# Optimization experiments

Measured on AMD Instinct MI355X. Metric: run time of the kernel, lower is better.

Reference implementation:

```python
import jax, jax.numpy as jnp
import numpy as np
from jax import lax

B = 2048
C = 8
H = W = 14
NP = H * W  # 196
DIM = 192
THETA = 0.7


def _unfold3(z):
    # z: [B, C, H, W] -> patches [B, C, 9, H, W], matching F.unfold(kernel=3, pad=1)
    p = jnp.pad(z, ((0, 0), (0, 0), (1, 1), (1, 1)))
    return jnp.stack([p[:, :, dy:dy + H, dx:dx + W]
                      for dy in range(3) for dx in range(3)], axis=2)


def setup_inputs() -> dict:
    key = jax.random.key(0)
    ks = jax.random.split(key, 10)
    s = 0.1
    return {
        "x": jax.random.normal(ks[0], (B, 1 + NP, DIM), dtype=jnp.float32),
        "W1": jax.random.normal(ks[1], (C, DIM), dtype=jnp.float32) * s,      # linear1 192->8
        "b1": jax.random.normal(ks[2], (C,), dtype=jnp.float32) * s,
        "conv1_w": jax.random.normal(ks[3], (C, C), dtype=jnp.float32) * s,   # 1x1 conv
        "conv1_b": jax.random.normal(ks[4], (C,), dtype=jnp.float32) * s,
        "cdc_w": jax.random.normal(ks[5], (C, C, 1, 5), dtype=jnp.float32) * s,
        "wc1": jax.random.normal(ks[6], (C, C), dtype=jnp.float32) * s,       # WConv1 (1x1)
        "wc2": jax.random.normal(ks[7], (C, C), dtype=jnp.float32) * s,       # WConv2 (1x1)
        "hist_w": jax.random.normal(ks[8], (DIM, C), dtype=jnp.float32) * s,  # linear 8->192
        "hist_b": jax.random.normal(ks[9], (DIM,), dtype=jnp.float32) * s,
    }


def reference(x, W1, b1, conv1_w, conv1_b, cdc_w, wc1, wc2, hist_w, hist_b):
    class_token, tok = x[:, :1, :], x[:, 1:, :]
    # linear1: [B,196,192] -> [B,196,8]
    t = jnp.einsum('bnd,cd->bnc', tok, W1) + b1
    # -> [B,8,14,14]
    t = t.reshape(-1, H, W, C).transpose(0, 3, 1, 2)

    # conv1 (1x1)
    x1 = jnp.einsum('bihw,oi->bohw', t, conv1_w) + conv1_b[None, :, None, None]

    # CDC: scatter the 1x5 weights into a 3x3 cross-shaped kernel
    w5 = cdc_w[:, :, 0, :]  # [O,I,5]
    z = jnp.zeros((C, C, 1), dtype=cdc_w.dtype)
    k9 = jnp.concatenate([z, w5[:, :, 0:1], z,
                          w5[:, :, 1:2], w5[:, :, 2:3], w5[:, :, 3:4],
                          z, w5[:, :, 4:5], z], axis=2).reshape(C, C, 3, 3)
    out_normal = lax.conv_general_dilated(
        t, k9, window_strides=(1, 1), padding=((1, 1), (1, 1)),
        dimension_numbers=('NCHW', 'OIHW', 'NCHW'))
    kernel_diff = cdc_w.sum(axis=(2, 3))  # [O,I]
    out_diff = jnp.einsum('bihw,oi->bohw', t, kernel_diff)
    x2 = out_normal - THETA * out_diff

    z_star = x1 + x2  # [B,8,14,14]

    # TokenHistogram
    mu = jnp.einsum('bihw,oi->bohw', z_star, wc1)
    gamma = jnp.einsum('bihw,oi->bohw', z_star, wc2)
    zp = _unfold3(z_star)   # [B,8,9,14,14]
    mp = _unfold3(mu)
    gp = _unfold3(gamma)
    u = gp * (zp - mp)
    z_hist = jnp.exp(-u * u).sum(axis=2) / 9.0  # [B,8,14,14]
    # torch .reshape(-1, NP, 8): plain row-major reshape (mixes C and HW)
    z_hist = z_hist.reshape(-1, NP, C)
    y = jnp.einsum('bnc,dc->bnd', z_hist, hist_w) + hist_b  # [B,196,192]

    return jnp.concatenate([class_token, y], axis=1)
```

## Files before the change

kernel.cpp:

```cpp
#include <hip/hip_runtime.h>


#define DIMD 192

__launch_bounds__(256)
__global__ void sadapter_kernel(
    const float* __restrict__ x,
    const float* __restrict__ W1,
    const float* __restrict__ b1,
    const float* __restrict__ conv1_w,
    const float* __restrict__ conv1_b,
    const float* __restrict__ cdc_w,
    const float* __restrict__ wc1,
    const float* __restrict__ wc2,
    const float* __restrict__ hist_w,
    const float* __restrict__ hist_b,
    float* __restrict__ out)
{
    __shared__ float smem[4608];
    float* TS  = smem;
    float* ZH  = smem;
    float* PS  = smem + 2048;
    float* WB2 = smem + 4096;

    const int tid = threadIdx.x;
    const float* xb   = x   + (size_t)blockIdx.x * (197 * DIMD);
    float*       outb = out + (size_t)blockIdx.x * (197 * DIMD);

    {
        float4 z4 = make_float4(0.f, 0.f, 0.f, 0.f);
        float4 o4 = make_float4(1.f, 1.f, 1.f, 1.f);
        ((float4*)TS)[tid]       = z4;
        ((float4*)TS)[tid + 256] = z4;
        ((float4*)PS)[tid]       = o4;
        ((float4*)PS)[tid + 256] = o4;
    }
    if (tid < 64) {
        const float* c5 = cdc_w + tid * 5;
        float k0 = c5[0], k1 = c5[1], k2 = c5[2], k3 = c5[3], k4 = c5[4];
        float kd = k0 + k1 + k2 + k3 + k4;
        float* wp = WB2 + tid * 8;
        wp[0] = conv1_w[tid] + k2 - 0.7f * kd;
        wp[1] = k0; wp[2] = k1; wp[3] = k3; wp[4] = k4;
        wp[5] = wc1[tid];
        wp[6] = wc2[tid];
        wp[7] = 0.f;
    }
    __syncthreads();

    if (tid < 196) {
        const float4* rowp = (const float4*)(xb + DIMD + tid * DIMD);
        float acc[8];
        #pragma unroll
        for (int c = 0; c < 8; ++c) acc[c] = b1[c];
        #pragma unroll
        for (int blk = 0; blk < 6; ++blk) {
            float4 tv[8];
            #pragma unroll
            for (int u = 0; u < 8; ++u) tv[u] = rowp[blk * 8 + u];
            #pragma unroll
            for (int c = 0; c < 8; ++c) {
                const float* wrow = W1 + c * DIMD + blk * 32;
                #pragma unroll
                for (int u = 0; u < 8; ++u) {
                    acc[c] += tv[u].x * wrow[u * 4 + 0] + tv[u].y * wrow[u * 4 + 1]
                            + tv[u].z * wrow[u * 4 + 2] + tv[u].w * wrow[u * 4 + 3];
                }
            }
        }
        int h = tid / 14, w = tid - h * 14;
        float* tp = TS + (h + 1) * 16 + (w + 1);
        #pragma unroll
        for (int c = 0; c < 8; ++c) tp[c * 256] = acc[c];
    } else if (tid >= 208) {
        ((float4*)outb)[tid - 208] = ((const float4*)xb)[tid - 208];
    }
    __syncthreads();

    if (tid < 196) {
        int h = tid / 14, w = tid - h * 14;
        const float* tp = TS + (h + 1) * 16 + (w + 1);
        float zv[8];
        #pragma unroll
        for (int c = 0; c < 8; ++c) zv[c] = conv1_b[c];
        #pragma unroll
        for (int i = 0; i < 8; ++i) {
            float t0 = tp[i * 256];
            float tu = tp[i * 256 - 16];
            float td = tp[i * 256 + 16];
            float tl = tp[i * 256 - 1];
            float tr = tp[i * 256 + 1];
            #pragma unroll
            for (int c = 0; c < 8; ++c) {
                const float* wp = WB2 + (c * 8 + i) * 8;
                float4 wv = *(const float4*)wp;
                float wd = wp[4];
                zv[c] += wv.x * t0 + wv.y * tu + wv.z * tl + wv.w * tr + wd * td;
            }
        }
        float* pp = PS + (h + 1) * 16 + (w + 1);
        #pragma unroll
        for (int c = 0; c < 8; ++c) {
            float mu = 0.f, ga = 0.f;
            #pragma unroll
            for (int i = 0; i < 8; ++i) {
                const float* wp = WB2 + (c * 8 + i) * 8;
                mu += wp[5] * zv[i];
                ga += wp[6] * zv[i];
            }
            float e = ga * (zv[c] - mu);
            pp[c * 256] = __expf(-e * e);
        }
    }
    __syncthreads();

    const int l  = tid & 63;
    const int wv = tid >> 6;
    const float4 ha0 = *(const float4*)(hist_w + l * 8);
    const float4 ha1 = *(const float4*)(hist_w + l * 8 + 4);
    const float4 hb0 = *(const float4*)(hist_w + (l + 64) * 8);
    const float4 hb1 = *(const float4*)(hist_w + (l + 64) * 8 + 4);
    const float4 hc0 = *(const float4*)(hist_w + (l + 128) * 8);
    const float4 hc1 = *(const float4*)(hist_w + (l + 128) * 8 + 4);
    const float  ba  = hist_b[l];
    const float  bb  = hist_b[l + 64];
    const float  bc  = hist_b[l + 128];

    if (tid < 196) {
        int h = tid / 14, w = tid - h * 14;
        const float* pb = PS + h * 16 + w;
        #pragma unroll
        for (int c = 0; c < 8; ++c) {
            const float* pr = pb + c * 256;
            float s9 = pr[0]  + pr[1]  + pr[2]
                     + pr[16] + pr[17] + pr[18]
                     + pr[32] + pr[33] + pr[34];
            ZH[c * 196 + tid] = s9 * (1.f / 9.f);
        }
    }
    __syncthreads();

    {
        float* oy = outb + DIMD;
        const int n2beg = wv * 49;
        #pragma unroll 2
        for (int k = 0; k < 49; ++k) {
            const int n2 = n2beg + k;
            const float4 z0 = *(const float4*)(ZH + n2 * 8);
            const float4 z1 = *(const float4*)(ZH + n2 * 8 + 4);
            float a0 = ba
                     + z0.x * ha0.x + z0.y * ha0.y + z0.z * ha0.z + z0.w * ha0.w
                     + z1.x * ha1.x + z1.y * ha1.y + z1.z * ha1.z + z1.w * ha1.w;
            float a1 = bb
                     + z0.x * hb0.x + z0.y * hb0.y + z0.z * hb0.z + z0.w * hb0.w
                     + z1.x * hb1.x + z1.y * hb1.y + z1.z * hb1.z + z1.w * hb1.w;
            float a2 = bc
                     + z0.x * hc0.x + z0.y * hc0.y + z0.z * hc0.z + z0.w * hc0.w
                     + z1.x * hc1.x + z1.y * hc1.y + z1.z * hc1.z + z1.w * hc1.w;
            float* orow = oy + n2 * DIMD;
            orow[l]       = a0;
            orow[l + 64]  = a1;
            orow[l + 128] = a2;
        }
    }
}

extern "C" void kernel_launch(void* const* d_in, const int* in_sizes, int n_in,
                              void* d_out, int out_size, void* d_ws, size_t ws_size,
                              hipStream_t stream)
{
    const float* x       = (const float*)d_in[0];
    const float* W1      = (const float*)d_in[1];
    const float* b1      = (const float*)d_in[2];
    const float* conv1_w = (const float*)d_in[3];
    const float* conv1_b = (const float*)d_in[4];
    const float* cdc_w   = (const float*)d_in[5];
    const float* wc1     = (const float*)d_in[6];
    const float* wc2     = (const float*)d_in[7];
    const float* hist_w  = (const float*)d_in[8];
    const float* hist_b  = (const float*)d_in[9];
    float* out = (float*)d_out;

    sadapter_kernel<<<2048, 256, 0, stream>>>(
        x, W1, b1, conv1_w, conv1_b, cdc_w, wc1, wc2, hist_w, hist_b, out);
}
```

Baseline: 152.8 us.

## Process two images per block, overlapping second image's loads with first's output writes

Each block now handles two batch images (b and b+1024) with half as many blocks. It interleaves the linear1 input reads of the second image with the histogram-projection output stores of the first, using nontemporal stores for the output. The aim is to overlap global loads with global stores inside one block and to spread the per-block setup cost over two images. In exchange there are fewer blocks (1024 for 256 CUs), more registers are live during the interleaved loop, and the second image's final phases run without any overlap.

New measurement: 167.0 us. 9.2% more time.

```diff
diff --git a/kernel.cpp b/kernel.cpp
--- a/kernel.cpp
+++ b/kernel.cpp
@@ -2,9 +2,73 @@
 
 
 #define DIMD 192
+#define IMGS 37824
+#define HB   1024
+
+typedef float vfloat4 __attribute__((ext_vector_type(4)));
+
+__device__ __forceinline__ void phase_bc(const float* __restrict__ TSrc,
+                                         float* __restrict__ Pdst,
+                                         const float* __restrict__ WB2,
+                                         const float* __restrict__ conv1_b,
+                                         int tid)
+{
+    if (tid < 196) {
+        int h = tid / 14, w = tid - h * 14;
+        const float* tp = TSrc + (h + 1) * 16 + (w + 1);
+        float zv[8];
+        #pragma unroll
+        for (int c = 0; c < 8; ++c) zv[c] = conv1_b[c];
+        #pragma unroll
+        for (int i = 0; i < 8; ++i) {
+            float t0 = tp[i * 256];
+            float tu = tp[i * 256 - 16];
+            float td = tp[i * 256 + 16];
+            float tl = tp[i * 256 - 1];
+            float tr = tp[i * 256 + 1];
+            #pragma unroll
+            for (int c = 0; c < 8; ++c) {
+                const float* wp = WB2 + (c * 8 + i) * 8;
+                float4 wv = *(const float4*)wp;
+                float wd = wp[4];
+                zv[c] += wv.x * t0 + wv.y * tu + wv.z * tl + wv.w * tr + wd * td;
+            }
+        }
+        float* pp = Pdst + (h + 1) * 16 + (w + 1);
+        #pragma unroll
+        for (int c = 0; c < 8; ++c) {
+            float mu = 0.f, ga = 0.f;
+            #pragma unroll
+            for (int i = 0; i < 8; ++i) {
+                const float* wp = WB2 + (c * 8 + i) * 8;
+                mu += wp[5] * zv[i];
+                ga += wp[6] * zv[i];
+            }
+            float e = ga * (zv[c] - mu);
+            pp[c * 256] = __expf(-e * e);
+        }
+    }
+}
+
+__device__ __forceinline__ void phase_c2(const float* __restrict__ Psrc,
+                                         float* __restrict__ ZHdst, int tid)
+{
+    if (tid < 196) {
+        int h = tid / 14, w = tid - h * 14;
+        const float* pb = Psrc + h * 16 + w;
+        #pragma unroll
+        for (int c = 0; c < 8; ++c) {
+            const float* pr = pb + c * 256;
+            float s9 = pr[0]  + pr[1]  + pr[2]
+                     + pr[16] + pr[17] + pr[18]
+                     + pr[32] + pr[33] + pr[34];
+            ZHdst[c * 196 + tid] = s9 * (1.f / 9.f);
+        }
+    }
+}
 
 __launch_bounds__(256)
-__global__ void sadapter_kernel(
+__global__ void sadapter_pipe(
     const float* __restrict__ x,
     const float* __restrict__ W1,
     const float* __restrict__ b1,
@@ -18,23 +82,23 @@
     float* __restrict__ out)
 {
     __shared__ float smem[4608];
-    float* TS  = smem;
-    float* ZH  = smem;
-    float* PS  = smem + 2048;
+    float* r1  = smem;
+    float* r2  = smem + 2048;
     float* WB2 = smem + 4096;
 
     const int tid = threadIdx.x;
-    const float* xb   = x   + (size_t)blockIdx.x * (197 * DIMD);
-    float*       outb = out + (size_t)blockIdx.x * (197 * DIMD);
-
-    {
-        float4 z4 = make_float4(0.f, 0.f, 0.f, 0.f);
-        float4 o4 = make_float4(1.f, 1.f, 1.f, 1.f);
-        ((float4*)TS)[tid]       = z4;
-        ((float4*)TS)[tid + 256] = z4;
-        ((float4*)PS)[tid]       = o4;
-        ((float4*)PS)[tid + 256] = o4;
-    }
+    const float* xb0 = x  + (size_t)blockIdx.x * IMGS;
+    const float* xb1 = xb0 + (size_t)HB * IMGS;
+    float* ob0 = out + (size_t)blockIdx.x * IMGS;
+    float* ob1 = ob0 + (size_t)HB * IMGS;
+
+    const float4 z4 = make_float4(0.f, 0.f, 0.f, 0.f);
+    const float4 o4 = make_float4(1.f, 1.f, 1.f, 1.f);
+
+    ((float4*)r1)[tid]       = z4;
+    ((float4*)r1)[tid + 256] = z4;
+    ((float4*)r2)[tid]       = o4;
+    ((float4*)r2)[tid + 256] = o4;
     if (tid < 64) {
         const float* c5 = cdc_w + tid * 5;
         float k0 = c5[0], k1 = c5[1], k2 = c5[2], k3 = c5[3], k4 = c5[4];
@@ -49,10 +113,10 @@
     __syncthreads();
 
     if (tid < 196) {
-        const float4* rowp = (const float4*)(xb + DIMD + tid * DIMD);
-        float acc[8];
-        #pragma unroll
-        for (int c = 0; c < 8; ++c) acc[c] = b1[c];
+        const float4* rowp = (const float4*)(xb0 + DIMD + tid * DIMD);
+        float acc0[8];
+        #pragma unroll
+        for (int c = 0; c < 8; ++c) acc0[c] = b1[c];
         #pragma unroll
         for (int blk = 0; blk < 6; ++blk) {
             float4 tv[8];
@@ -63,57 +127,32 @@
                 const float* wrow = W1 + c * DIMD + blk * 32;
                 #pragma unroll
                 for (int u = 0; u < 8; ++u) {
-                    acc[c] += tv[u].x * wrow[u * 4 + 0] + tv[u].y * wrow[u * 4 + 1]
-                            + tv[u].z * wrow[u * 4 + 2] + tv[u].w * wrow[u * 4 + 3];
+                    acc0[c] += tv[u].x * wrow[u * 4 + 0] + tv[u].y * wrow[u * 4 + 1]
+                             + tv[u].z * wrow[u * 4 + 2] + tv[u].w * wrow[u * 4 + 3];
                 }
             }
         }
         int h = tid / 14, w = tid - h * 14;
-        float* tp = TS + (h + 1) * 16 + (w + 1);
-        #pragma unroll
-        for (int c = 0; c < 8; ++c) tp[c * 256] = acc[c];
-    } else if (tid >= 208) {
-        ((float4*)outb)[tid - 208] = ((const float4*)xb)[tid - 208];
-    }
-    __syncthreads();
-
-    if (tid < 196) {
-        int h = tid / 14, w = tid - h * 14;
-        const float* tp = TS + (h + 1) * 16 + (w + 1);
-        float zv[8];
-        #pragma unroll
-        for (int c = 0; c < 8; ++c) zv[c] = conv1_b[c];
-        #pragma unroll
-        for (int i = 0; i < 8; ++i) {
-            float t0 = tp[i * 256];
-            float tu = tp[i * 256 - 16];
-            float td = tp[i * 256 + 16];
-            float tl = tp[i * 256 - 1];
-            float tr = tp[i * 256 + 1];
-            #pragma unroll
-            for (int c = 0; c < 8; ++c) {
-                const float* wp = WB2 + (c * 8 + i) * 8;
-                float4 wv = *(const float4*)wp;
-                float wd = wp[4];
-                zv[c] += wv.x * t0 + wv.y * tu + wv.z * tl + wv.w * tr + wd * td;
-            }
-        }
-        float* pp = PS + (h + 1) * 16 + (w + 1);
-        #pragma unroll
-        for (int c = 0; c < 8; ++c) {
-            float mu = 0.f, ga = 0.f;
-            #pragma unroll
-            for (int i = 0; i < 8; ++i) {
-                const float* wp = WB2 + (c * 8 + i) * 8;
-                mu += wp[5] * zv[i];
-                ga += wp[6] * zv[i];
-            }
-            float e = ga * (zv[c] - mu);
-            pp[c * 256] = __expf(-e * e);
-        }
-    }
-    __syncthreads();
-
+        float* tp = r1 + (h + 1) * 16 + (w + 1);
+        #pragma unroll
+        for (int c = 0; c < 8; ++c) tp[c * 256] = acc0[c];
+    } else {
+        for (int f = tid - 196; f < 96; f += 60) {
+            int img = f / 48, j = f - img * 48;
+            const vfloat4 v = ((const vfloat4*)(img ? xb1 : xb0))[j];
+            __builtin_nontemporal_store(v, ((vfloat4*)(img ? ob1 : ob0)) + j);
+        }
+    }
+    __syncthreads();
+
+    phase_bc(r1, r2, WB2, conv1_b, tid);
+    __syncthreads();
+
+    phase_c2(r2, r1, tid);
+    __syncthreads();
+
+    ((float4*)r2)[tid]       = z4;
+    ((float4*)r2)[tid + 256] = z4;
     const int l  = tid & 63;
     const int wv = tid >> 6;
     const float4 ha0 = *(const float4*)(hist_w + l * 8);
@@ -124,43 +163,99 @@
     const float4 hc1 = *(const float4*)(hist_w + (l + 128) * 8 + 4);
     const float  ba  = hist_b[l];
     const float  bb  = hist_b[l + 64];
-    const float  bc  = hist_b[l + 128];
-
-    if (tid < 196) {
-        int h = tid / 14, w = tid - h * 14;
-        const float* pb = PS + h * 16 + w;
-        #pragma unroll
-        for (int c = 0; c < 8; ++c) {
-            const float* pr = pb + c * 256;
-            float s9 = pr[0]  + pr[1]  + pr[2]
-                     + pr[16] + pr[17] + pr[18]
-                     + pr[32] + pr[33] + pr[34];
-            ZH[c * 196 + tid] = s9 * (1.f / 9.f);
-        }
-    }
-    __syncthreads();
-
+    const float  bc_ = hist_b[l + 128];
+    const int n2beg = wv * 49;
+    __syncthreads();
+
+    float acc[8];
+    #pragma unroll
+    for (int c = 0; c < 8; ++c) acc[c] = b1[c];
     {
-        float* oy = outb + DIMD;
-        const int n2beg = wv * 49;
+        const float4* rowp1 = (const float4*)(xb1 + DIMD + tid * DIMD);
+        float* oy0 = ob0 + DIMD;
+        for (int s = 0; s < 12; ++s) {
+            if (tid < 196) {
+                float4 t0 = rowp1[s * 4 + 0];
+                float4 t1 = rowp1[s * 4 + 1];
+                float4 t2 = rowp1[s * 4 + 2];
+                float4 t3 = rowp1[s * 4 + 3];
+                #pragma unroll
+                for (int c = 0; c < 8; ++c) {
+                    const float* wr = W1 + c * DIMD + s * 16;
+                    acc[c] += t0.x * wr[0]  + t0.y * wr[1]  + t0.z * wr[2]  + t0.w * wr[3]
+                            + t1.x * wr[4]  + t1.y * wr[5]  + t1.z * wr[6]  + t1.w * wr[7]
+                            + t2.x * wr[8]  + t2.y * wr[9]  + t2.z * wr[10] + t2.w * wr[11]
+                            + t3.x * wr[12] + t3.y * wr[13] + t3.z * wr[14] + t3.w * wr[15];
+                }
+            }
+            #pragma unroll
+            for (int k = 0; k < 4; ++k) {
+                const int n2 = n2beg + s * 4 + k;
+                const float4 z0 = *(const float4*)(r1 + n2 * 8);
+                const float4 z1 = *(const float4*)(r1 + n2 * 8 + 4);
+                float a0 = ba + z0.x*ha0.x + z0.y*ha0.y + z0.z*ha0.z + z0.w*ha0.w
+                              + z1.x*ha1.x + z1.y*ha1.y + z1.z*ha1.z + z1.w*ha1.w;
+                float a1 = bb + z0.x*hb0.x + z0.y*hb0.y + z0.z*hb0.z + z0.w*hb0.w
+                              + z1.x*hb1.x + z1.y*hb1.y + z1.z*hb1.z + z1.w*hb1.w;
+                float a2 = bc_+ z0.x*hc0.x + z0.y*hc0.y + z0.z*hc0.z + z0.w*hc0.w
+                              + z1.x*hc1.x + z1.y*hc1.y + z1.z*hc1.z + z1.w*hc1.w;
+                float* orow = oy0 + n2 * DIMD;
+                __builtin_nontemporal_store(a0, orow + l);
+                __builtin_nontemporal_store(a1, orow + l + 64);
+                __builtin_nontemporal_store(a2, orow + l + 128);
+            }
+        }
+        {
+            const int n2 = n2beg + 48;
+            const float4 z0 = *(const float4*)(r1 + n2 * 8);
+            const float4 z1 = *(const float4*)(r1 + n2 * 8 + 4);
+            float a0 = ba + z0.x*ha0.x + z0.y*ha0.y + z0.z*ha0.z + z0.w*ha0.w
+                          + z1.x*ha1.x + z1.y*ha1.y + z1.z*ha1.z + z1.w*ha1.w;
+            float a1 = bb + z0.x*hb0.x + z0.y*hb0.y + z0.z*hb0.z + z0.w*hb0.w
+                          + z1.x*hb1.x + z1.y*hb1.y + z1.z*hb1.z + z1.w*hb1.w;
+            float a2 = bc_+ z0.x*hc0.x + z0.y*hc0.y + z0.z*hc0.z + z0.w*hc0.w
+                          + z1.x*hc1.x + z1.y*hc1.y + z1.z*hc1.z + z1.w*hc1.w;
+            float* orow = oy0 + n2 * DIMD;
+            __builtin_nontemporal_store(a0, orow + l);
+            __builtin_nontemporal_store(a1, orow + l + 64);
+            __builtin_nontemporal_store(a2, orow + l + 128);
+        }
+    }
+    __syncthreads();
+
+    ((float4*)r1)[tid]       = o4;
+    ((float4*)r1)[tid + 256] = o4;
+    if (tid < 196) {
+        int h = tid / 14, w = tid - h * 14;
+        float* tp = r2 + (h + 1) * 16 + (w + 1);
+        #pragma unroll
+        for (int c = 0; c < 8; ++c) tp[c * 256] = acc[c];
+    }
+    __syncthreads();
+
+    phase_bc(r2, r1, WB2, conv1_b, tid);
+    __syncthreads();
+
+    phase_c2(r1, r2, tid);
+    __syncthreads();
+
+    {
+        float* oy1 = ob1 + DIMD;
         #pragma unroll 2
         for (int k = 0; k < 49; ++k) {
             const int n2 = n2beg + k;
-            const float4 z0 = *(const float4*)(ZH + n2 * 8);
-            const float4 z1 = *(const float4*)(ZH + n2 * 8 + 4);
-            float a0 = ba
-                     + z0.x * ha0.x + z0.y * ha0.y + z0.z * ha0.z + z0.w * ha0.w
-                     + z1.x * ha1.x + z1.y * ha1.y + z1.z * ha1.z + z1.w * ha1.w;
-            float a1 = bb
-                     + z0.x * hb0.x + z0.y * hb0.y + z0.z * hb0.z + z0.w * hb0.w
-                     + z1.x * hb1.x + z1.y * hb1.y + z1.z * hb1.z + z1.w * hb1.w;
-            float a2 = bc
-                     + z0.x * hc0.x + z0.y * hc0.y + z0.z * hc0.z + z0.w * hc0.w
-                     + z1.x * hc1.x + z1.y * hc1.y + z1.z * hc1.z + z1.w * hc1.w;
-            float* orow = oy + n2 * DIMD;
-            orow[l]       = a0;
-            orow[l + 64]  = a1;
-            orow[l + 128] = a2;
+            const float4 z0 = *(const float4*)(r2 + n2 * 8);
+            const float4 z1 = *(const float4*)(r2 + n2 * 8 + 4);
+            float a0 = ba + z0.x*ha0.x + z0.y*ha0.y + z0.z*ha0.z + z0.w*ha0.w
+                          + z1.x*ha1.x + z1.y*ha1.y + z1.z*ha1.z + z1.w*ha1.w;
+            float a1 = bb + z0.x*hb0.x + z0.y*hb0.y + z0.z*hb0.z + z0.w*hb0.w
+                          + z1.x*hb1.x + z1.y*hb1.y + z1.z*hb1.z + z1.w*hb1.w;
+            float a2 = bc_+ z0.x*hc0.x + z0.y*hc0.y + z0.z*hc0.z + z0.w*hc0.w
+                          + z1.x*hc1.x + z1.y*hc1.y + z1.z*hc1.z + z1.w*hc1.w;
+            float* orow = oy1 + n2 * DIMD;
+            __builtin_nontemporal_store(a0, orow + l);
+            __builtin_nontemporal_store(a1, orow + l + 64);
+            __builtin_nontemporal_store(a2, orow + l + 128);
         }
     }
 }
@@ -181,6 +276,6 @@
     const float* hist_b  = (const float*)d_in[9];
     float* out = (float*)d_out;
 
-    sadapter_kernel<<<2048, 256, 0, stream>>>(
+    sadapter_pipe<<<1024, 256, 0, stream>>>(
         x, W1, b1, conv1_w, conv1_b, cdc_w, wc1, wc2, hist_w, hist_b, out);
 }
```
